# Kernel optimization log

Hardware: AMD Instinct MI355X
Metric: run time of the kernel (lower is better)

The kernel has to match this reference:

```python
import jax, jax.numpy as jnp
import numpy as np

N_NODES = 20000
EPS_BN = 1e-5
NEG_SLOPE = 0.2


def gat_conv(x, W, att_src, att_dst, bias, src, dst, heads, out_ch, concat):
    n = x.shape[0]
    h = (x @ W).reshape(n, heads, out_ch)                       # [N,H,C]
    a_src = jnp.sum(h * att_src, axis=-1)                       # [N,H]
    a_dst = jnp.sum(h * att_dst, axis=-1)                       # [N,H]
    e = jax.nn.leaky_relu(a_src[src] + a_dst[dst], NEG_SLOPE)   # [E,H]
    # segment softmax over incoming edges of each destination node
    m = jax.ops.segment_max(e, dst, num_segments=n)             # [N,H]
    e = jnp.exp(e - m[dst])
    denom = jax.ops.segment_sum(e, dst, num_segments=n)         # [N,H]
    alpha = e / (denom[dst] + 1e-16)                            # [E,H]
    msg = alpha[:, :, None] * h[src]                            # [E,H,C]
    out = jax.ops.segment_sum(msg, dst, num_segments=n)         # [N,H,C]
    if concat:
        out = out.reshape(n, heads * out_ch)
    else:
        out = out.mean(axis=1)
    return out + bias


def batch_norm(x, gamma, beta):
    mu = x.mean(axis=0)
    var = x.var(axis=0)  # biased, matches torch normalization
    return (x - mu) * jax.lax.rsqrt(var + EPS_BN) * gamma + beta


def setup_inputs() -> dict:
    key = jax.random.key(0)
    ks = jax.random.split(key, 16)
    n, d_in, hid, heads = N_NODES, 768, 128, 8
    n_edges = 160000
    x = jax.random.normal(ks[0], (n, d_in), dtype=jnp.float32)
    edge_index = jax.random.randint(ks[1], (2, n_edges), 0, n, dtype=jnp.int64)
    s = lambda fi, fo: (2.0 / (fi + fo)) ** 0.5
    return {
        "x": x,
        "edge_index": edge_index,
        "W1": jax.random.normal(ks[2], (d_in, heads * hid), jnp.float32) * s(d_in, heads * hid),
        "att_src1": jax.random.normal(ks[3], (heads, hid), jnp.float32) * 0.1,
        "att_dst1": jax.random.normal(ks[4], (heads, hid), jnp.float32) * 0.1,
        "bias1": jnp.zeros((heads * hid,), jnp.float32),
        "bn1_g": jnp.ones((heads * hid,), jnp.float32),
        "bn1_b": jnp.zeros((heads * hid,), jnp.float32),
        "W2": jax.random.normal(ks[5], (heads * hid, hid), jnp.float32) * s(heads * hid, hid),
        "att_src2": jax.random.normal(ks[6], (1, hid), jnp.float32) * 0.1,
        "att_dst2": jax.random.normal(ks[7], (1, hid), jnp.float32) * 0.1,
        "bias2": jnp.zeros((hid,), jnp.float32),
        "bn2_g": jnp.ones((hid,), jnp.float32),
        "bn2_b": jnp.zeros((hid,), jnp.float32),
        "Wc1": jax.random.normal(ks[8], (hid, 64), jnp.float32) * s(hid, 64),
        "bc1": jnp.zeros((64,), jnp.float32),
        "Wc2": jax.random.normal(ks[9], (64, 2), jnp.float32) * s(64, 2),
        "bc2": jnp.zeros((2,), jnp.float32),
    }


def reference(x, edge_index, W1, att_src1, att_dst1, bias1, bn1_g, bn1_b,
              W2, att_src2, att_dst2, bias2, bn2_g, bn2_b,
              Wc1, bc1, Wc2, bc2):
    n = x.shape[0]
    # PyG GATConv default: add self-loops
    loops = jnp.arange(n, dtype=edge_index.dtype)
    src = jnp.concatenate([edge_index[0], loops])
    dst = jnp.concatenate([edge_index[1], loops])

    h = gat_conv(x, W1, att_src1, att_dst1, bias1, src, dst, heads=8, out_ch=128, concat=True)
    h = jax.nn.elu(batch_norm(h, bn1_g, bn1_b))
    # dropout disabled (deterministic reference)
    h = gat_conv(h, W2, att_src2, att_dst2, bias2, src, dst, heads=1, out_ch=128, concat=False)
    h = jax.nn.elu(batch_norm(h, bn2_g, bn2_b))
    h = jax.nn.elu(h @ Wc1 + bc1)
    return h @ Wc2 + bc2  # [N, 2] logits
```

## Files before the change

### kernel.cpp

```cpp
#include <hip/hip_runtime.h>
#include <stdint.h>

typedef unsigned short u16;
typedef __bf16 bf16x8 __attribute__((ext_vector_type(8)));
typedef float f32x4 __attribute__((ext_vector_type(4)));

__device__ __forceinline__ float b2f(u16 u) {
    unsigned x = ((unsigned)u) << 16;
    return __builtin_bit_cast(float, x);
}
__device__ __forceinline__ u16 f2b(float f) {
    unsigned x = __builtin_bit_cast(unsigned, f);
    x = x + 0x7fffu + ((x >> 16) & 1u);
    return (u16)(x >> 16);
}
__device__ __forceinline__ float leaky(float v) { return v > 0.f ? v : 0.2f * v; }
__device__ __forceinline__ float elu(float v) { return v > 0.f ? v : expm1f(v); }

__device__ __forceinline__ void gload16(const u16* g, u16* l) {
    __builtin_amdgcn_global_load_lds((const __attribute__((address_space(1))) void*)(const void*)g,
                                     (__attribute__((address_space(3))) void*)(void*)l, 16, 0, 0);
}

__global__ void k_init(const int* __restrict__ ei, int* __restrict__ flag,
                       int* __restrict__ deg, int E0, int N) {
    for (int i = blockIdx.x * blockDim.x + threadIdx.x; i < N; i += gridDim.x * blockDim.x)
        deg[i] = 0;
    if (blockIdx.x == 0) {
        if (threadIdx.x == 0) *flag = 0;
        __syncthreads();
        int lim = E0 < 4096 ? E0 : 4096;
        int any = 0;
        for (int i = threadIdx.x; i < lim; i += 256) any |= (ei[2 * i + 1] != 0);
        if (any) atomicOr(flag, 1);
    }
}

__global__ void k_cast4(const float* __restrict__ in, u16* __restrict__ out, size_t n4) {
    size_t i = blockIdx.x * (size_t)blockDim.x + threadIdx.x;
    size_t stride = (size_t)gridDim.x * blockDim.x;
    for (; i < n4; i += stride) {
        float4 v = ((const float4*)in)[i];
        ushort4 o;
        o.x = f2b(v.x); o.y = f2b(v.y); o.z = f2b(v.z); o.w = f2b(v.w);
        ((ushort4*)out)[i] = o;
    }
}

__global__ void k_tcast2(const float* __restrict__ W1, u16* __restrict__ w1t,
                         const float* __restrict__ W2, u16* __restrict__ w2t) {
    __shared__ float tile[32][33];
    int bid = blockIdx.x;
    const float* in; u16* outp; int R, C, cx, ry;
    if (bid < 768) { in = W1; outp = w1t; R = 768; C = 1024; cx = bid & 31; ry = bid >> 5; }
    else { int b = bid - 768; in = W2; outp = w2t; R = 1024; C = 128; cx = b & 3; ry = b >> 2; }
    int tx = threadIdx.x & 31, ty = threadIdx.x >> 5;
    int c0 = cx * 32, r0 = ry * 32;
    #pragma unroll
    for (int i = 0; i < 32; i += 8)
        tile[ty + i][tx] = in[(size_t)(r0 + ty + i) * C + c0 + tx];
    __syncthreads();
    #pragma unroll
    for (int i = 0; i < 32; i += 8)
        outp[(size_t)(c0 + ty + i) * R + r0 + tx] = f2b(tile[tx][ty + i]);
}

#define GBM 128
#define GBN 128
#define GBK 64
#define LDT 72
#define SPLITK 4

__global__ __launch_bounds__(256) void k_gemm(const u16* __restrict__ A, const u16* __restrict__ Bt,
                                              u16* __restrict__ C, int M, int NN, int K, int nCB) {
    __shared__ __align__(16) u16 As[GBM][GBK];
    __shared__ __align__(16) u16 Bs[GBN][GBK];
    int nwg = gridDim.x, orig = blockIdx.x;
    int q = nwg >> 3, r8 = nwg & 7, xcd = orig & 7, sub = orig >> 3;
    int wgid = (xcd < r8 ? xcd * (q + 1) : r8 * (q + 1) + (xcd - r8) * q) + sub;
    int rb = wgid / nCB, cb = wgid % nCB;
    int brow = rb * GBM, bcol = cb * GBN;

    int t = threadIdx.x, lane = t & 63, wid = t >> 6;
    int wm = (wid >> 1) * 64, wn = (wid & 1) * 64;
    int fr = lane & 15, fq = lane >> 4;
    f32x4 acc[4][4] = {};
    int srow = lane >> 3;
    int scol = (((lane & 7) ^ srow)) * 8;
    int dcol = (lane & 7) * 8;
    int nK = K / GBK;
    for (int kt = 0; kt < nK; ++kt) {
        int k0 = kt * GBK;
        #pragma unroll
        for (int cc = 0; cc < 8; ++cc) {
            int c = wid * 8 + cc;
            int r = (c & 15) * 8 + srow;
            if (c < 16) gload16(A + (size_t)(brow + r) * K + k0 + scol, &As[r][dcol]);
            else        gload16(Bt + (size_t)(bcol + r) * K + k0 + scol, &Bs[r][dcol]);
        }
        __syncthreads();
        #pragma unroll
        for (int kk = 0; kk < 2; ++kk) {
            int ko = kk * 32 + fq * 8;
            int kos = ko ^ ((fr & 7) << 3);
            bf16x8 af[4], bg[4];
            #pragma unroll
            for (int i = 0; i < 4; ++i) {
                af[i] = *reinterpret_cast<const bf16x8*>(&As[wm + i * 16 + fr][kos]);
                bg[i] = *reinterpret_cast<const bf16x8*>(&Bs[wn + i * 16 + fr][kos]);
            }
            #pragma unroll
            for (int mi = 0; mi < 4; ++mi)
                #pragma unroll
                for (int ni = 0; ni < 4; ++ni)
                    acc[mi][ni] = __builtin_amdgcn_mfma_f32_16x16x32_bf16(af[mi], bg[ni], acc[mi][ni], 0, 0, 0);
        }
        __syncthreads();
    }
    #pragma unroll
    for (int mi = 0; mi < 4; ++mi) {
        #pragma unroll
        for (int j = 0; j < 4; ++j) {
            int row = brow + wm + mi * 16 + fq * 4 + j;
            if (row < M) {
                #pragma unroll
                for (int ni = 0; ni < 4; ++ni) {
                    int col = bcol + wn + ni * 16 + fr;
                    C[(size_t)row * NN + col] = f2b(acc[mi][ni][j]);
                }
            }
        }
    }
}

__global__ __launch_bounds__(256) void k_gemm2(const u16* __restrict__ A, const u16* __restrict__ Bt,
                                               float* __restrict__ Cp, int M, int K,
                                               const float* __restrict__ scA, const float* __restrict__ shA) {
    __shared__ __align__(16) u16 As[GBM][LDT];
    __shared__ __align__(16) u16 Bs[GBN][LDT];
    int brow = blockIdx.x * GBM;
    int ks = blockIdx.y;
    int kBase = ks * (K / SPLITK);
    int t = threadIdx.x;
    int lane = t & 63, wid = t >> 6;
    int wm = (wid >> 1) * 64, wn = (wid & 1) * 64;
    int fr = lane & 15, fq = lane >> 4;
    f32x4 acc[4][4] = {};
    int tr = t >> 3, tc = (t & 7) * 8;
    const int nK = 1024 / SPLITK / GBK;
    for (int kt = 0; kt < nK; ++kt) {
        int k0 = kBase + kt * GBK;
        #pragma unroll
        for (int rr = 0; rr < 4; ++rr) {
            int r = tr + rr * 32;
            int grow = brow + r;
            uint4 bv = *reinterpret_cast<const uint4*>(Bt + (size_t)r * K + k0 + tc);
            *reinterpret_cast<uint4*>(&Bs[r][tc]) = bv;
            uint4 av = make_uint4(0, 0, 0, 0);
            if (grow < M) {
                uint4 u = *reinterpret_cast<const uint4*>(A + (size_t)grow * K + k0 + tc);
                float4 s0 = *(const float4*)(scA + k0 + tc);
                float4 s1 = *(const float4*)(scA + k0 + tc + 4);
                float4 h0 = *(const float4*)(shA + k0 + tc);
                float4 h1 = *(const float4*)(shA + k0 + tc + 4);
                u16 w0 = f2b(elu(b2f((u16)(u.x & 0xffff)) * s0.x + h0.x));
                u16 w1 = f2b(elu(b2f((u16)(u.x >> 16))    * s0.y + h0.y));
                u16 w2 = f2b(elu(b2f((u16)(u.y & 0xffff)) * s0.z + h0.z));
                u16 w3 = f2b(elu(b2f((u16)(u.y >> 16))    * s0.w + h0.w));
                u16 w4 = f2b(elu(b2f((u16)(u.z & 0xffff)) * s1.x + h1.x));
                u16 w5 = f2b(elu(b2f((u16)(u.z >> 16))    * s1.y + h1.y));
                u16 w6 = f2b(elu(b2f((u16)(u.w & 0xffff)) * s1.z + h1.z));
                u16 w7 = f2b(elu(b2f((u16)(u.w >> 16))    * s1.w + h1.w));
                av.x = (unsigned)w0 | ((unsigned)w1 << 16);
                av.y = (unsigned)w2 | ((unsigned)w3 << 16);
                av.z = (unsigned)w4 | ((unsigned)w5 << 16);
                av.w = (unsigned)w6 | ((unsigned)w7 << 16);
            }
            *reinterpret_cast<uint4*>(&As[r][tc]) = av;
        }
        __syncthreads();
        #pragma unroll
        for (int kk = 0; kk < 2; ++kk) {
            int ko = kk * 32 + fq * 8;
            bf16x8 af[4], bg[4];
            #pragma unroll
            for (int i = 0; i < 4; ++i) {
                af[i] = *reinterpret_cast<const bf16x8*>(&As[wm + i * 16 + fr][ko]);
                bg[i] = *reinterpret_cast<const bf16x8*>(&Bs[wn + i * 16 + fr][ko]);
            }
            #pragma unroll
            for (int mi = 0; mi < 4; ++mi)
                #pragma unroll
                for (int ni = 0; ni < 4; ++ni)
                    acc[mi][ni] = __builtin_amdgcn_mfma_f32_16x16x32_bf16(af[mi], bg[ni], acc[mi][ni], 0, 0, 0);
        }
        __syncthreads();
    }
    float* base = Cp + (size_t)ks * M * 128;
    #pragma unroll
    for (int mi = 0; mi < 4; ++mi) {
        #pragma unroll
        for (int j = 0; j < 4; ++j) {
            int row = brow + wm + mi * 16 + fq * 4 + j;
            if (row < M) {
                #pragma unroll
                for (int ni = 0; ni < 4; ++ni) {
                    int col = wn + ni * 16 + fr;
                    base[(size_t)row * 128 + col] = acc[mi][ni][j];
                }
            }
        }
    }
}

__global__ __launch_bounds__(256) void k_red2(const float* __restrict__ Cp,
                                              const float* __restrict__ attS, const float* __restrict__ attD,
                                              u16* __restrict__ h2b, float* __restrict__ asrc,
                                              float* __restrict__ adst, int M) {
    int t = threadIdx.x, lane = t & 63, wid = t >> 6;
    int row = blockIdx.x * 4 + wid;
    if (row >= M) return;
    int c = lane * 2;
    float s0 = 0.f, s1 = 0.f;
    #pragma unroll
    for (int s = 0; s < SPLITK; ++s) {
        float2 v = *(const float2*)(Cp + ((size_t)s * M + row) * 128 + c);
        s0 += v.x; s1 += v.y;
    }
    ushort2 o; o.x = f2b(s0); o.y = f2b(s1);
    *(ushort2*)(h2b + (size_t)row * 128 + c) = o;
    float ps = s0 * attS[c] + s1 * attS[c + 1];
    float pd = s0 * attD[c] + s1 * attD[c + 1];
    #pragma unroll
    for (int m = 1; m < 64; m <<= 1) { ps += __shfl_xor(ps, m); pd += __shfl_xor(pd, m); }
    if (lane == 0) { asrc[row] = ps; adst[row] = pd; }
}

__global__ void k_att8(const u16* __restrict__ h, const float* __restrict__ attS,
                       const float* __restrict__ attD, float* __restrict__ asrc,
                       float* __restrict__ adst, int N) {
    int t = threadIdx.x;
    int half = t >> 7, i = t & 127;
    int row = blockIdx.x * 2 + half;
    if (row >= N) return;
    int head = i >> 4, g = i & 15;
    const u16* hp = h + (size_t)row * 1024 + head * 128 + g * 8;
    const float* sp = attS + head * 128 + g * 8;
    const float* dp = attD + head * 128 + g * 8;
    ushort4 u0 = *(const ushort4*)hp;
    ushort4 u1 = *(const ushort4*)(hp + 4);
    float hv[8] = {b2f(u0.x), b2f(u0.y), b2f(u0.z), b2f(u0.w),
                   b2f(u1.x), b2f(u1.y), b2f(u1.z), b2f(u1.w)};
    float ps = 0.f, pd = 0.f;
    #pragma unroll
    for (int j = 0; j < 8; ++j) { ps += hv[j] * sp[j]; pd += hv[j] * dp[j]; }
    #pragma unroll
    for (int m = 1; m < 16; m <<= 1) { ps += __shfl_xor(ps, m); pd += __shfl_xor(pd, m); }
    if (g == 0) { asrc[row * 8 + head] = ps; adst[row * 8 + head] = pd; }
}

__global__ void k_deg(const int* __restrict__ ei, const int* __restrict__ flag,
                      int* __restrict__ deg, int E0, int E) {
    bool i64 = (*flag == 0);
    for (int e = blockIdx.x * blockDim.x + threadIdx.x; e < E; e += gridDim.x * blockDim.x) {
        int d;
        if (e < E0) d = i64 ? ei[2 * (E0 + e)] : ei[E0 + e];
        else d = e - E0;
        atomicAdd(&deg[d], 1);
    }
}

__global__ __launch_bounds__(1024) void k_scan(const int* __restrict__ deg, int* __restrict__ off,
                                               int* __restrict__ cursor, int n) {
    __shared__ int part[1024];
    int t = threadIdx.x;
    int chunk = (n + 1023) >> 10;
    int beg = t * chunk, end = beg + chunk;
    if (end > n) end = n;
    int s = 0;
    for (int i = beg; i < end; ++i) s += deg[i];
    part[t] = s;
    __syncthreads();
    for (int d = 1; d < 1024; d <<= 1) {
        int v = (t >= d) ? part[t - d] : 0;
        __syncthreads();
        part[t] += v;
        __syncthreads();
    }
    int run = (t == 0) ? 0 : part[t - 1];
    for (int i = beg; i < end; ++i) { off[i] = run; cursor[i] = run; run += deg[i]; }
    if (t == 1023) off[n] = part[1023];
}

__global__ void k_scatter(const int* __restrict__ ei, const int* __restrict__ flag,
                          int* __restrict__ cursor, int* __restrict__ csr, int E0, int E) {
    bool i64 = (*flag == 0);
    for (int e = blockIdx.x * blockDim.x + threadIdx.x; e < E; e += gridDim.x * blockDim.x) {
        int s, d;
        if (e < E0) {
            if (i64) { s = ei[2 * e]; d = ei[2 * (E0 + e)]; }
            else     { s = ei[e];     d = ei[E0 + e]; }
        } else { s = d = e - E0; }
        int pos = atomicAdd(&cursor[d], 1);
        csr[pos] = s;
    }
}

__global__ __launch_bounds__(256) void k_agg1(const int* __restrict__ off, const int* __restrict__ csr,
                                              const float* __restrict__ asrc, const float* __restrict__ adst,
                                              const u16* __restrict__ h1, u16* __restrict__ outg, int N) {
    __shared__ float pch[64][8];
    __shared__ float invs[8];
    int node = blockIdx.x;
    if (node >= N) return;
    int t = threadIdx.x, lane = t & 63, wid = t >> 6;
    int hh = t >> 5;
    int c0 = t * 4;
    int lo = off[node], hi = off[node + 1];
    float ad_l = 0.f, mmax = -1e30f, ssum = 0.f;
    int h = lane & 7, es = lane >> 3;
    if (wid == 0) {
        ad_l = adst[(size_t)node * 8 + h];
        for (int i = lo + es; i < hi; i += 8)
            mmax = fmaxf(mmax, leaky(asrc[(size_t)csr[i] * 8 + h] + ad_l));
        #pragma unroll
        for (int mask = 8; mask < 64; mask <<= 1) mmax = fmaxf(mmax, __shfl_xor(mmax, mask));
    }
    float a0 = 0.f, a1 = 0.f, a2 = 0.f, a3 = 0.f;
    for (int base = lo; base < hi; base += 64) {
        int cend = base + 64 < hi ? base + 64 : hi;
        if (wid == 0) {
            for (int i = base + es; i < cend; i += 8) {
                float p = __expf(leaky(asrc[(size_t)csr[i] * 8 + h] + ad_l) - mmax);
                pch[i - base][h] = p;
                ssum += p;
            }
        }
        __syncthreads();
        for (int i = base; i < cend; ++i) {
            float p = pch[i - base][hh];
            ushort4 u = *(const ushort4*)(h1 + (size_t)csr[i] * 1024 + c0);
            a0 += p * b2f(u.x); a1 += p * b2f(u.y);
            a2 += p * b2f(u.z); a3 += p * b2f(u.w);
        }
        __syncthreads();
    }
    if (wid == 0) {
        #pragma unroll
        for (int mask = 8; mask < 64; mask <<= 1) ssum += __shfl_xor(ssum, mask);
        if (lane < 8) invs[lane] = 1.f / (ssum + 1e-16f);
    }
    __syncthreads();
    float inv = invs[hh];
    ushort4 o;
    o.x = f2b(a0 * inv); o.y = f2b(a1 * inv); o.z = f2b(a2 * inv); o.w = f2b(a3 * inv);
    *(ushort4*)(outg + (size_t)node * 1024 + c0) = o;
}

__global__ __launch_bounds__(128) void k_agg2(const int* __restrict__ off, const int* __restrict__ csr,
                                              const float* __restrict__ asrc, const float* __restrict__ adst,
                                              const u16* __restrict__ h2, u16* __restrict__ outg, int N) {
    __shared__ float pch[64];
    __shared__ float invsh;
    int node = blockIdx.x;
    if (node >= N) return;
    int t = threadIdx.x, lane = t & 63, wid = t >> 6;
    int lo = off[node], hi = off[node + 1];
    float ad = adst[node];
    float mmax = -1e30f, ssum = 0.f;
    if (wid == 0) {
        for (int i = lo + lane; i < hi; i += 64)
            mmax = fmaxf(mmax, leaky(asrc[csr[i]] + ad));
        #pragma unroll
        for (int mask = 1; mask < 64; mask <<= 1) mmax = fmaxf(mmax, __shfl_xor(mmax, mask));
    }
    float acc = 0.f;
    for (int base = lo; base < hi; base += 64) {
        int cend = base + 64 < hi ? base + 64 : hi;
        if (wid == 0 && base + lane < cend) {
            float p = __expf(leaky(asrc[csr[base + lane]] + ad) - mmax);
            pch[lane] = p;
            ssum += p;
        }
        __syncthreads();
        for (int i = base; i < cend; ++i)
            acc += pch[i - base] * b2f(h2[(size_t)csr[i] * 128 + t]);
        __syncthreads();
    }
    if (wid == 0) {
        #pragma unroll
        for (int mask = 1; mask < 64; mask <<= 1) ssum += __shfl_xor(ssum, mask);
        if (lane == 0) invsh = 1.f / (ssum + 1e-16f);
    }
    __syncthreads();
    outg[(size_t)node * 128 + t] = f2b(acc * invsh);
}

template <int CH>
__global__ __launch_bounds__(256) void k_bnpart(const u16* __restrict__ g, float* __restrict__ ps,
                                                float* __restrict__ ps2, int Nrows, int rowsPerChunk) {
    const int TPR = CH / 4;
    const int RPI = 256 / TPR;
    int t = threadIdx.x;
    int rl = t / TPR, c4 = (t % TPR) * 4;
    int chunk = blockIdx.x;
    int r0 = chunk * rowsPerChunk;
    int r1 = r0 + rowsPerChunk; if (r1 > Nrows) r1 = Nrows;
    float s[4] = {0.f, 0.f, 0.f, 0.f}, s2[4] = {0.f, 0.f, 0.f, 0.f};
    for (int r = r0 + rl; r < r1; r += RPI) {
        ushort4 u = *(const ushort4*)(g + (size_t)r * CH + c4);
        float v0 = b2f(u.x), v1 = b2f(u.y), v2 = b2f(u.z), v3 = b2f(u.w);
        s[0] += v0; s2[0] += v0 * v0;
        s[1] += v1; s2[1] += v1 * v1;
        s[2] += v2; s2[2] += v2 * v2;
        s[3] += v3; s2[3] += v3 * v3;
    }
    size_t prow = (size_t)(chunk * RPI + rl) * CH + c4;
    *(float4*)(ps + prow)  = make_float4(s[0], s[1], s[2], s[3]);
    *(float4*)(ps2 + prow) = make_float4(s2[0], s2[1], s2[2], s2[3]);
}

__global__ __launch_bounds__(256) void k_bnfinal(const float* __restrict__ ps, const float* __restrict__ ps2,
                                                 const float* __restrict__ gamma, const float* __restrict__ beta,
                                                 float* __restrict__ scale, float* __restrict__ shift,
                                                 int P, int CH, int Nrows) {
    int t = threadIdx.x, lane = t & 63, wid = t >> 6;
    int col = blockIdx.x * 4 + wid;
    if (col >= CH) return;
    float s = 0.f, s2 = 0.f;
    for (int p = lane; p < P; p += 64) {
        s += ps[(size_t)p * CH + col];
        s2 += ps2[(size_t)p * CH + col];
    }
    #pragma unroll
    for (int m = 1; m < 64; m <<= 1) { s += __shfl_xor(s, m); s2 += __shfl_xor(s2, m); }
    if (lane == 0) {
        double mu = (double)s / Nrows;
        double var = (double)s2 / Nrows - mu * mu;
        if (var < 0) var = 0;
        float sc = gamma[col] * rsqrtf((float)var + 1e-5f);
        scale[col] = sc;
        shift[col] = beta[col] - (float)mu * sc;
    }
}

__global__ __launch_bounds__(256) void k_cls(const u16* __restrict__ g2raw,
                                             const float* __restrict__ scale2, const float* __restrict__ shift2,
                                             const float* __restrict__ Wc1, const float* __restrict__ bc1,
                                             const float* __restrict__ Wc2, const float* __restrict__ bc2,
                                             float* __restrict__ out, int N) {
    __shared__ float wl[128 * 64];
    __shared__ float hs[4][128];
    int t = threadIdx.x, lane = t & 63, wid = t >> 6;
    for (int i = t; i < 128 * 64; i += 256) wl[i] = Wc1[i];
    float sc0 = scale2[2 * lane], sc1 = scale2[2 * lane + 1];
    float sh0 = shift2[2 * lane], sh1 = shift2[2 * lane + 1];
    float bb = bc1[lane];
    float c2a = Wc2[lane * 2], c2b = Wc2[lane * 2 + 1];
    float o2a = bc2[0], o2b = bc2[1];
    __syncthreads();
    int row0 = blockIdx.x * 64;
    for (int it = 0; it < 16; ++it) {
        int row = row0 + it * 4 + wid;
        if (row >= N) continue;
        const u16* hp = g2raw + (size_t)row * 128 + 2 * lane;
        float y0 = b2f(hp[0]) * sc0 + sh0; y0 = y0 > 0.f ? y0 : expm1f(y0);
        float y1 = b2f(hp[1]) * sc1 + sh1; y1 = y1 > 0.f ? y1 : expm1f(y1);
        hs[wid][2 * lane] = y0;
        hs[wid][2 * lane + 1] = y1;
        float tj = bb;
        #pragma unroll 8
        for (int c = 0; c < 128; ++c) tj += hs[wid][c] * wl[c * 64 + lane];
        tj = tj > 0.f ? tj : expm1f(tj);
        float v0 = tj * c2a, v1 = tj * c2b;
        #pragma unroll
        for (int m = 1; m < 64; m <<= 1) { v0 += __shfl_xor(v0, m); v1 += __shfl_xor(v1, m); }
        if (lane == 0) {
            out[(size_t)row * 2 + 0] = v0 + o2a;
            out[(size_t)row * 2 + 1] = v1 + o2b;
        }
    }
}

extern "C" void kernel_launch(void* const* d_in, const int* in_sizes, int n_in,
                              void* d_out, int out_size, void* d_ws, size_t ws_size,
                              hipStream_t stream) {
    const float* x     = (const float*)d_in[0];
    const int*   ei    = (const int*)d_in[1];
    const float* W1    = (const float*)d_in[2];
    const float* attS1 = (const float*)d_in[3];
    const float* attD1 = (const float*)d_in[4];
    const float* bn1g  = (const float*)d_in[6];
    const float* bn1b  = (const float*)d_in[7];
    const float* W2    = (const float*)d_in[8];
    const float* attS2 = (const float*)d_in[9];
    const float* attD2 = (const float*)d_in[10];
    const float* bn2g  = (const float*)d_in[12];
    const float* bn2b  = (const float*)d_in[13];
    const float* Wc1   = (const float*)d_in[14];
    const float* bc1   = (const float*)d_in[15];
    const float* Wc2   = (const float*)d_in[16];
    const float* bc2   = (const float*)d_in[17];
    float* out = (float*)d_out;

    const int DIN = 768, F1 = 1024, C2 = 128;
    const int N = in_sizes[0] / DIN;
    const int E0 = in_sizes[1] / 2;
    const int E = E0 + N;
    const int nMB = (N + GBM - 1) / GBM;
    const int Mp = nMB * GBM;

    char* w = (char*)d_ws;
    auto take = [&](size_t bytes) -> void* {
        void* p = (void*)w;
        w += (bytes + 255) & ~(size_t)255;
        return p;
    };
    u16* xb     = (u16*)take((size_t)Mp * DIN * 2);
    u16* bufA   = (u16*)take((size_t)N * F1 * 2);
    u16* h1b    = (u16*)take((size_t)N * F1 * 2);
    u16* w1t    = (u16*)take((size_t)F1 * DIN * 2);
    u16* w2t    = (u16*)take((size_t)C2 * F1 * 2);
    float* asrc1 = (float*)take((size_t)N * 8 * 4);
    float* adst1 = (float*)take((size_t)N * 8 * 4);
    int* deg    = (int*)take((size_t)N * 4);
    int* off    = (int*)take((size_t)(N + 1) * 4);
    int* cursor = (int*)take((size_t)N * 4);
    int* csr    = (int*)take((size_t)E * 4);
    int* flag   = (int*)take(256);
    u16* h2b    = (u16*)take((size_t)N * C2 * 2);
    float* asrc2 = (float*)take((size_t)N * 4);
    float* adst2 = (float*)take((size_t)N * 4);
    u16* g2     = (u16*)take((size_t)N * C2 * 2);
    float* scale1 = (float*)take(F1 * 4);
    float* shift1 = (float*)take(F1 * 4);
    float* scale2 = (float*)take(C2 * 4);
    float* shift2 = (float*)take(C2 * 4);
    float* psA   = (float*)take((size_t)1024 * 1024 * 4);
    float* psB   = (float*)take((size_t)1024 * 1024 * 4);
    float* part  = (float*)h1b;

    k_init<<<64, 256, 0, stream>>>(ei, flag, deg, E0, N);
    k_cast4<<<2048, 256, 0, stream>>>(x, xb, (size_t)N * DIN / 4);
    k_tcast2<<<768 + 128, 256, 0, stream>>>(W1, w1t, W2, w2t);

    k_gemm<<<nMB * (F1 / GBN), 256, 0, stream>>>(xb, w1t, h1b, N, F1, DIN, F1 / GBN);
    k_att8<<<(N + 1) / 2, 256, 0, stream>>>(h1b, attS1, attD1, asrc1, adst1, N);

    k_deg<<<512, 256, 0, stream>>>(ei, flag, deg, E0, E);
    k_scan<<<1, 1024, 0, stream>>>(deg, off, cursor, N);
    k_scatter<<<512, 256, 0, stream>>>(ei, flag, cursor, csr, E0, E);

    k_agg1<<<N, 256, 0, stream>>>(off, csr, asrc1, adst1, h1b, bufA, N);
    {
        int nchunk = 256, rpc = (N + nchunk - 1) / nchunk;
        k_bnpart<1024><<<nchunk, 256, 0, stream>>>(bufA, psA, psB, N, rpc);
        k_bnfinal<<<F1 / 4, 256, 0, stream>>>(psA, psB, bn1g, bn1b, scale1, shift1, nchunk, F1, N);
    }

    k_gemm2<<<dim3(nMB, SPLITK), 256, 0, stream>>>(bufA, w2t, part, N, F1, scale1, shift1);
    k_red2<<<(N + 3) / 4, 256, 0, stream>>>(part, attS2, attD2, h2b, asrc2, adst2, N);

    k_agg2<<<N, 128, 0, stream>>>(off, csr, asrc2, adst2, h2b, g2, N);
    {
        int nchunk = 128, rpc = (N + nchunk - 1) / nchunk;
        k_bnpart<128><<<nchunk, 256, 0, stream>>>(g2, psA, psB, N, rpc);
        k_bnfinal<<<C2 / 4, 256, 0, stream>>>(psA, psB, bn2g, bn2b, scale2, shift2, nchunk * 8, C2, N);
    }

    k_cls<<<(N + 63) / 64, 256, 0, stream>>>(g2, scale2, shift2, Wc1, bc1, Wc2, bc2, out, N);
}
```

Measured before the change: 345.8 us.

## Merge preprocessing, CSR build, and batch-norm stats into fewer cooperative kernels

Merges the init, cast, and transpose-cast kernels into one launch. Builds the CSR (degree count, scan, scatter) inside a single cooperative kernel using grid syncs and a parallel block-level scan instead of a single-block scan. Fuses each batch-norm partial and final reduction into one cooperative kernel. The goal is fewer launches and less serial scan time, at the cost of grid-wide barriers and cooperative-launch limits on resident blocks (79 blocks for the CSR kernel).

```diff
diff --git a/kernel.cpp b/kernel.cpp
--- a/kernel.cpp
+++ b/kernel.cpp
@@ -1,5 +1,8 @@
 #include <hip/hip_runtime.h>
+#include <hip/hip_cooperative_groups.h>
 #include <stdint.h>
+
+namespace cg = cooperative_groups;
 
 typedef unsigned short u16;
 typedef __bf16 bf16x8 __attribute__((ext_vector_type(8)));
@@ -22,47 +25,107 @@
                                      (__attribute__((address_space(3))) void*)(void*)l, 16, 0, 0);
 }
 
-__global__ void k_init(const int* __restrict__ ei, int* __restrict__ flag,
-                       int* __restrict__ deg, int E0, int N) {
-    for (int i = blockIdx.x * blockDim.x + threadIdx.x; i < N; i += gridDim.x * blockDim.x)
-        deg[i] = 0;
-    if (blockIdx.x == 0) {
-        if (threadIdx.x == 0) *flag = 0;
-        __syncthreads();
-        int lim = E0 < 4096 ? E0 : 4096;
-        int any = 0;
-        for (int i = threadIdx.x; i < lim; i += 256) any |= (ei[2 * i + 1] != 0);
-        if (any) atomicOr(flag, 1);
-    }
-}
-
-__global__ void k_cast4(const float* __restrict__ in, u16* __restrict__ out, size_t n4) {
-    size_t i = blockIdx.x * (size_t)blockDim.x + threadIdx.x;
-    size_t stride = (size_t)gridDim.x * blockDim.x;
-    for (; i < n4; i += stride) {
-        float4 v = ((const float4*)in)[i];
-        ushort4 o;
-        o.x = f2b(v.x); o.y = f2b(v.y); o.z = f2b(v.z); o.w = f2b(v.w);
-        ((ushort4*)out)[i] = o;
-    }
-}
-
-__global__ void k_tcast2(const float* __restrict__ W1, u16* __restrict__ w1t,
-                         const float* __restrict__ W2, u16* __restrict__ w2t) {
-    __shared__ float tile[32][33];
-    int bid = blockIdx.x;
-    const float* in; u16* outp; int R, C, cx, ry;
-    if (bid < 768) { in = W1; outp = w1t; R = 768; C = 1024; cx = bid & 31; ry = bid >> 5; }
-    else { int b = bid - 768; in = W2; outp = w2t; R = 1024; C = 128; cx = b & 3; ry = b >> 2; }
-    int tx = threadIdx.x & 31, ty = threadIdx.x >> 5;
-    int c0 = cx * 32, r0 = ry * 32;
-    #pragma unroll
-    for (int i = 0; i < 32; i += 8)
-        tile[ty + i][tx] = in[(size_t)(r0 + ty + i) * C + c0 + tx];
+__global__ void k_pre(const float* __restrict__ x, u16* __restrict__ xb,
+                      const float* __restrict__ W1, u16* __restrict__ w1t,
+                      const float* __restrict__ W2, u16* __restrict__ w2t,
+                      const int* __restrict__ ei, int* __restrict__ flag,
+                      int* __restrict__ deg, size_t n4, int E0, int N) {
+    int bid = blockIdx.x, t = threadIdx.x;
+    if (bid < 2048) {
+        size_t i = (size_t)bid * 256 + t;
+        const size_t stride = (size_t)2048 * 256;
+        for (size_t k = i; k < n4; k += stride) {
+            float4 v = ((const float4*)x)[k];
+            ushort4 o;
+            o.x = f2b(v.x); o.y = f2b(v.y); o.z = f2b(v.z); o.w = f2b(v.w);
+            ((ushort4*)xb)[k] = o;
+        }
+        for (size_t k = i; k < (size_t)N; k += stride) deg[k] = 0;
+        if (bid == 0) {
+            if (t == 0) *flag = 0;
+            __syncthreads();
+            int lim = E0 < 4096 ? E0 : 4096;
+            int any = 0;
+            for (int k = t; k < lim; k += 256) any |= (ei[2 * k + 1] != 0);
+            if (any) atomicOr(flag, 1);
+        }
+    } else {
+        __shared__ float tile[32][33];
+        int b = bid - 2048;
+        const float* in; u16* outp; int R, C, cx, ry;
+        if (b < 768) { in = W1; outp = w1t; R = 768; C = 1024; cx = b & 31; ry = b >> 5; }
+        else { int b2 = b - 768; in = W2; outp = w2t; R = 1024; C = 128; cx = b2 & 3; ry = b2 >> 2; }
+        int tx = t & 31, ty = t >> 5;
+        int c0 = cx * 32, r0 = ry * 32;
+        #pragma unroll
+        for (int i = 0; i < 32; i += 8)
+            tile[ty + i][tx] = in[(size_t)(r0 + ty + i) * C + c0 + tx];
+        __syncthreads();
+        #pragma unroll
+        for (int i = 0; i < 32; i += 8)
+            outp[(size_t)(c0 + ty + i) * R + r0 + tx] = f2b(tile[tx][ty + i]);
+    }
+}
+
+__global__ __launch_bounds__(256) void k_csr(const int* __restrict__ ei, const int* __restrict__ flag,
+                                             int* __restrict__ deg, int* __restrict__ off,
+                                             int* __restrict__ cursor, int* __restrict__ csr,
+                                             int* __restrict__ bsum, int* __restrict__ bbase,
+                                             int E0, int E, int N) {
+    cg::grid_group grid = cg::this_grid();
+    __shared__ int s[256];
+    int t = threadIdx.x, b = blockIdx.x;
+    int gid = b * 256 + t, gsz = gridDim.x * 256;
+    bool i64 = (*flag == 0);
+    for (int e = gid; e < E; e += gsz) {
+        int d;
+        if (e < E0) d = i64 ? ei[2 * (E0 + e)] : ei[E0 + e];
+        else d = e - E0;
+        atomicAdd(&deg[d], 1);
+    }
+    grid.sync();
+    int idx = gid;
+    int v = (idx < N) ? deg[idx] : 0;
+    s[t] = v;
     __syncthreads();
     #pragma unroll
-    for (int i = 0; i < 32; i += 8)
-        outp[(size_t)(c0 + ty + i) * R + r0 + tx] = f2b(tile[tx][ty + i]);
+    for (int d = 1; d < 256; d <<= 1) {
+        int x = (t >= d) ? s[t - d] : 0;
+        __syncthreads();
+        s[t] += x;
+        __syncthreads();
+    }
+    int incl = s[t];
+    if (t == 255) bsum[b] = incl;
+    grid.sync();
+    if (b == 0) {
+        int nb = gridDim.x;
+        int bv = (t < nb) ? bsum[t] : 0;
+        s[t] = bv;
+        __syncthreads();
+        #pragma unroll
+        for (int d = 1; d < 256; d <<= 1) {
+            int x = (t >= d) ? s[t - d] : 0;
+            __syncthreads();
+            s[t] += x;
+            __syncthreads();
+        }
+        if (t < nb) bbase[t] = s[t] - bv;
+        if (t == 0) off[N] = E;
+    }
+    grid.sync();
+    int excl = bbase[b] + incl - v;
+    if (idx < N) { off[idx] = excl; cursor[idx] = excl; }
+    grid.sync();
+    for (int e = gid; e < E; e += gsz) {
+        int sv, d;
+        if (e < E0) {
+            if (i64) { sv = ei[2 * e]; d = ei[2 * (E0 + e)]; }
+            else     { sv = ei[e];     d = ei[E0 + e]; }
+        } else { sv = d = e - E0; }
+        int pos = atomicAdd(&cursor[d], 1);
+        csr[pos] = sv;
+    }
 }
 
 #define GBM 128
@@ -259,53 +322,6 @@
     if (g == 0) { asrc[row * 8 + head] = ps; adst[row * 8 + head] = pd; }
 }
 
-__global__ void k_deg(const int* __restrict__ ei, const int* __restrict__ flag,
-                      int* __restrict__ deg, int E0, int E) {
-    bool i64 = (*flag == 0);
-    for (int e = blockIdx.x * blockDim.x + threadIdx.x; e < E; e += gridDim.x * blockDim.x) {
-        int d;
-        if (e < E0) d = i64 ? ei[2 * (E0 + e)] : ei[E0 + e];
-        else d = e - E0;
-        atomicAdd(&deg[d], 1);
-    }
-}
-
-__global__ __launch_bounds__(1024) void k_scan(const int* __restrict__ deg, int* __restrict__ off,
-                                               int* __restrict__ cursor, int n) {
-    __shared__ int part[1024];
-    int t = threadIdx.x;
-    int chunk = (n + 1023) >> 10;
-    int beg = t * chunk, end = beg + chunk;
-    if (end > n) end = n;
-    int s = 0;
-    for (int i = beg; i < end; ++i) s += deg[i];
-    part[t] = s;
-    __syncthreads();
-    for (int d = 1; d < 1024; d <<= 1) {
-        int v = (t >= d) ? part[t - d] : 0;
-        __syncthreads();
-        part[t] += v;
-        __syncthreads();
-    }
-    int run = (t == 0) ? 0 : part[t - 1];
-    for (int i = beg; i < end; ++i) { off[i] = run; cursor[i] = run; run += deg[i]; }
-    if (t == 1023) off[n] = part[1023];
-}
-
-__global__ void k_scatter(const int* __restrict__ ei, const int* __restrict__ flag,
-                          int* __restrict__ cursor, int* __restrict__ csr, int E0, int E) {
-    bool i64 = (*flag == 0);
-    for (int e = blockIdx.x * blockDim.x + threadIdx.x; e < E; e += gridDim.x * blockDim.x) {
-        int s, d;
-        if (e < E0) {
-            if (i64) { s = ei[2 * e]; d = ei[2 * (E0 + e)]; }
-            else     { s = ei[e];     d = ei[E0 + e]; }
-        } else { s = d = e - E0; }
-        int pos = atomicAdd(&cursor[d], 1);
-        csr[pos] = s;
-    }
-}
-
 __global__ __launch_bounds__(256) void k_agg1(const int* __restrict__ off, const int* __restrict__ csr,
                                               const float* __restrict__ asrc, const float* __restrict__ adst,
                                               const u16* __restrict__ h1, u16* __restrict__ outg, int N) {
@@ -396,51 +412,92 @@
     outg[(size_t)node * 128 + t] = f2b(acc * invsh);
 }
 
-template <int CH>
-__global__ __launch_bounds__(256) void k_bnpart(const u16* __restrict__ g, float* __restrict__ ps,
-                                                float* __restrict__ ps2, int Nrows, int rowsPerChunk) {
-    const int TPR = CH / 4;
-    const int RPI = 256 / TPR;
+__global__ __launch_bounds__(256) void k_bn1(const u16* __restrict__ g, const float* __restrict__ gamma,
+                                             const float* __restrict__ beta, float* __restrict__ ps,
+                                             float* __restrict__ ps2, float* __restrict__ scale,
+                                             float* __restrict__ shift, int Nrows) {
+    cg::grid_group grid = cg::this_grid();
     int t = threadIdx.x;
-    int rl = t / TPR, c4 = (t % TPR) * 4;
+    int c4 = t * 4;
     int chunk = blockIdx.x;
-    int r0 = chunk * rowsPerChunk;
-    int r1 = r0 + rowsPerChunk; if (r1 > Nrows) r1 = Nrows;
-    float s[4] = {0.f, 0.f, 0.f, 0.f}, s2[4] = {0.f, 0.f, 0.f, 0.f};
-    for (int r = r0 + rl; r < r1; r += RPI) {
-        ushort4 u = *(const ushort4*)(g + (size_t)r * CH + c4);
+    int rpc = (Nrows + gridDim.x - 1) / gridDim.x;
+    int r0 = chunk * rpc;
+    int r1 = r0 + rpc; if (r1 > Nrows) r1 = Nrows;
+    float s[4] = {0.f, 0.f, 0.f, 0.f}, q[4] = {0.f, 0.f, 0.f, 0.f};
+    for (int r = r0; r < r1; ++r) {
+        ushort4 u = *(const ushort4*)(g + (size_t)r * 1024 + c4);
         float v0 = b2f(u.x), v1 = b2f(u.y), v2 = b2f(u.z), v3 = b2f(u.w);
-        s[0] += v0; s2[0] += v0 * v0;
-        s[1] += v1; s2[1] += v1 * v1;
-        s[2] += v2; s2[2] += v2 * v2;
-        s[3] += v3; s2[3] += v3 * v3;
-    }
-    size_t prow = (size_t)(chunk * RPI + rl) * CH + c4;
-    *(float4*)(ps + prow)  = make_float4(s[0], s[1], s[2], s[3]);
-    *(float4*)(ps2 + prow) = make_float4(s2[0], s2[1], s2[2], s2[3]);
-}
-
-__global__ __launch_bounds__(256) void k_bnfinal(const float* __restrict__ ps, const float* __restrict__ ps2,
-                                                 const float* __restrict__ gamma, const float* __restrict__ beta,
-                                                 float* __restrict__ scale, float* __restrict__ shift,
-                                                 int P, int CH, int Nrows) {
-    int t = threadIdx.x, lane = t & 63, wid = t >> 6;
+        s[0] += v0; q[0] += v0 * v0;
+        s[1] += v1; q[1] += v1 * v1;
+        s[2] += v2; q[2] += v2 * v2;
+        s[3] += v3; q[3] += v3 * v3;
+    }
+    *(float4*)(ps + (size_t)chunk * 1024 + c4)  = make_float4(s[0], s[1], s[2], s[3]);
+    *(float4*)(ps2 + (size_t)chunk * 1024 + c4) = make_float4(q[0], q[1], q[2], q[3]);
+    grid.sync();
+    int lane = t & 63, wid = t >> 6;
     int col = blockIdx.x * 4 + wid;
-    if (col >= CH) return;
-    float s = 0.f, s2 = 0.f;
+    float fs = 0.f, fq = 0.f;
+    int P = gridDim.x;
     for (int p = lane; p < P; p += 64) {
-        s += ps[(size_t)p * CH + col];
-        s2 += ps2[(size_t)p * CH + col];
-    }
-    #pragma unroll
-    for (int m = 1; m < 64; m <<= 1) { s += __shfl_xor(s, m); s2 += __shfl_xor(s2, m); }
+        fs += ps[(size_t)p * 1024 + col];
+        fq += ps2[(size_t)p * 1024 + col];
+    }
+    #pragma unroll
+    for (int m = 1; m < 64; m <<= 1) { fs += __shfl_xor(fs, m); fq += __shfl_xor(fq, m); }
     if (lane == 0) {
-        double mu = (double)s / Nrows;
-        double var = (double)s2 / Nrows - mu * mu;
+        double mu = (double)fs / Nrows;
+        double var = (double)fq / Nrows - mu * mu;
         if (var < 0) var = 0;
         float sc = gamma[col] * rsqrtf((float)var + 1e-5f);
         scale[col] = sc;
         shift[col] = beta[col] - (float)mu * sc;
+    }
+}
+
+__global__ __launch_bounds__(256) void k_bn2(const u16* __restrict__ g, const float* __restrict__ gamma,
+                                             const float* __restrict__ beta, float* __restrict__ ps,
+                                             float* __restrict__ ps2, float* __restrict__ scale,
+                                             float* __restrict__ shift, int Nrows) {
+    cg::grid_group grid = cg::this_grid();
+    int t = threadIdx.x;
+    int rl = t >> 5, c4 = (t & 31) * 4;
+    int chunk = blockIdx.x;
+    int rpc = (Nrows + gridDim.x - 1) / gridDim.x;
+    int r0 = chunk * rpc;
+    int r1 = r0 + rpc; if (r1 > Nrows) r1 = Nrows;
+    float s[4] = {0.f, 0.f, 0.f, 0.f}, q[4] = {0.f, 0.f, 0.f, 0.f};
+    for (int r = r0 + rl; r < r1; r += 8) {
+        ushort4 u = *(const ushort4*)(g + (size_t)r * 128 + c4);
+        float v0 = b2f(u.x), v1 = b2f(u.y), v2 = b2f(u.z), v3 = b2f(u.w);
+        s[0] += v0; q[0] += v0 * v0;
+        s[1] += v1; q[1] += v1 * v1;
+        s[2] += v2; q[2] += v2 * v2;
+        s[3] += v3; q[3] += v3 * v3;
+    }
+    size_t prow = (size_t)(chunk * 8 + rl) * 128 + c4;
+    *(float4*)(ps + prow)  = make_float4(s[0], s[1], s[2], s[3]);
+    *(float4*)(ps2 + prow) = make_float4(q[0], q[1], q[2], q[3]);
+    grid.sync();
+    int lane = t & 63, wid = t >> 6;
+    if (wid == 0) {
+        int col = blockIdx.x;
+        int P = gridDim.x * 8;
+        float fs = 0.f, fq = 0.f;
+        for (int p = lane; p < P; p += 64) {
+            fs += ps[(size_t)p * 128 + col];
+            fq += ps2[(size_t)p * 128 + col];
+        }
+        #pragma unroll
+        for (int m = 1; m < 64; m <<= 1) { fs += __shfl_xor(fs, m); fq += __shfl_xor(fq, m); }
+        if (lane == 0) {
+            double mu = (double)fs / Nrows;
+            double var = (double)fq / Nrows - mu * mu;
+            if (var < 0) var = 0;
+            float sc = gamma[col] * rsqrtf((float)var + 1e-5f);
+            scale[col] = sc;
+            shift[col] = beta[col] - (float)mu * sc;
+        }
     }
 }
 
@@ -504,9 +561,9 @@
     float* out = (float*)d_out;
 
     const int DIN = 768, F1 = 1024, C2 = 128;
-    const int N = in_sizes[0] / DIN;
-    const int E0 = in_sizes[1] / 2;
-    const int E = E0 + N;
+    int N = in_sizes[0] / DIN;
+    int E0 = in_sizes[1] / 2;
+    int E = E0 + N;
     const int nMB = (N + GBM - 1) / GBM;
     const int Mp = nMB * GBM;
 
@@ -528,6 +585,8 @@
     int* cursor = (int*)take((size_t)N * 4);
     int* csr    = (int*)take((size_t)E * 4);
     int* flag   = (int*)take(256);
+    int* bsum   = (int*)take(256 * 4);
+    int* bbase  = (int*)take(256 * 4);
     u16* h2b    = (u16*)take((size_t)N * C2 * 2);
     float* asrc2 = (float*)take((size_t)N * 4);
     float* adst2 = (float*)take((size_t)N * 4);
@@ -540,22 +599,23 @@
     float* psB   = (float*)take((size_t)1024 * 1024 * 4);
     float* part  = (float*)h1b;
 
-    k_init<<<64, 256, 0, stream>>>(ei, flag, deg, E0, N);
-    k_cast4<<<2048, 256, 0, stream>>>(x, xb, (size_t)N * DIN / 4);
-    k_tcast2<<<768 + 128, 256, 0, stream>>>(W1, w1t, W2, w2t);
+    size_t n4 = (size_t)N * DIN / 4;
+
+    k_pre<<<2048 + 896, 256, 0, stream>>>(x, xb, W1, w1t, W2, w2t, ei, flag, deg, n4, E0, N);
+
+    {
+        int NB = (N + 255) / 256;
+        void* args[] = {&ei, &flag, &deg, &off, &cursor, &csr, &bsum, &bbase, &E0, &E, &N};
+        hipLaunchCooperativeKernel(reinterpret_cast<void*>(k_csr), dim3(NB), dim3(256), args, 0, stream);
+    }
 
     k_gemm<<<nMB * (F1 / GBN), 256, 0, stream>>>(xb, w1t, h1b, N, F1, DIN, F1 / GBN);
     k_att8<<<(N + 1) / 2, 256, 0, stream>>>(h1b, attS1, attD1, asrc1, adst1, N);
 
-    k_deg<<<512, 256, 0, stream>>>(ei, flag, deg, E0, E);
-    k_scan<<<1, 1024, 0, stream>>>(deg, off, cursor, N);
-    k_scatter<<<512, 256, 0, stream>>>(ei, flag, cursor, csr, E0, E);
-
     k_agg1<<<N, 256, 0, stream>>>(off, csr, asrc1, adst1, h1b, bufA, N);
     {
-        int nchunk = 256, rpc = (N + nchunk - 1) / nchunk;
-        k_bnpart<1024><<<nchunk, 256, 0, stream>>>(bufA, psA, psB, N, rpc);
-        k_bnfinal<<<F1 / 4, 256, 0, stream>>>(psA, psB, bn1g, bn1b, scale1, shift1, nchunk, F1, N);
+        void* args[] = {&bufA, &bn1g, &bn1b, &psA, &psB, &scale1, &shift1, &N};
+        hipLaunchCooperativeKernel(reinterpret_cast<void*>(k_bn1), dim3(256), dim3(256), args, 0, stream);
     }
 
     k_gemm2<<<dim3(nMB, SPLITK), 256, 0, stream>>>(bufA, w2t, part, N, F1, scale1, shift1);
@@ -563,9 +623,8 @@
 
     k_agg2<<<N, 128, 0, stream>>>(off, csr, asrc2, adst2, h2b, g2, N);
     {
-        int nchunk = 128, rpc = (N + nchunk - 1) / nchunk;
-        k_bnpart<128><<<nchunk, 256, 0, stream>>>(g2, psA, psB, N, rpc);
-        k_bnfinal<<<C2 / 4, 256, 0, stream>>>(psA, psB, bn2g, bn2b, scale2, shift2, nchunk * 8, C2, N);
+        void* args[] = {&g2, &bn2g, &bn2b, &psA, &psB, &scale2, &shift2, &N};
+        hipLaunchCooperativeKernel(reinterpret_cast<void*>(k_bn2), dim3(128), dim3(256), args, 0, stream);
     }
 
     k_cls<<<(N + 63) / 64, 256, 0, stream>>>(g2, scale2, shift2, Wc1, bc1, Wc2, bc2, out, N);
```

New measurement: 432.9 us. +25.2%, slower.
